# Kernel optimization log

Hardware: AMD Instinct MI355X
Metric: run time of the kernel (lower is better)

The kernel has to match this reference:

```python
import jax, jax.numpy as jnp
import numpy as np
from jax import lax

T, B, D, H = 256, 32, 768, 768


def setup_inputs() -> dict:
    key = jax.random.key(0)
    ks = jax.random.split(key, 8)
    s = 1.0 / np.sqrt(H)
    x = jax.random.normal(ks[0], (T, B, D), dtype=jnp.float32)
    h0 = jax.random.normal(ks[1], (2, B, H), dtype=jnp.float32) * s
    wih_f = jax.random.normal(ks[2], (3 * H, D), dtype=jnp.float32) * s
    whh_f = jax.random.normal(ks[3], (3 * H, H), dtype=jnp.float32) * s
    wih_b = jax.random.normal(ks[4], (3 * H, D), dtype=jnp.float32) * s
    whh_b = jax.random.normal(ks[5], (3 * H, H), dtype=jnp.float32) * s
    bih_f = jnp.zeros((3 * H,), jnp.float32)
    bhh_f = jnp.zeros((3 * H,), jnp.float32)
    bih_b = jnp.zeros((3 * H,), jnp.float32)
    bhh_b = jnp.zeros((3 * H,), jnp.float32)
    # sorted-descending lengths in [T//2, T], as PackedSequence requires
    lengths = jnp.sort(jax.random.randint(ks[6], (B,), T // 2, T + 1))[::-1].astype(jnp.int32)
    return dict(x=x, h0=h0, wih_f=wih_f, whh_f=whh_f, bih_f=bih_f, bhh_f=bhh_f,
                wih_b=wih_b, whh_b=whh_b, bih_b=bih_b, bhh_b=bhh_b, lengths=lengths)


def _gru_scan(x_seq, h0d, Wih, Whh, bih, bhh, mask):
    """Masked GRU scan. x_seq [T,B,D], mask [T,B] bool; hidden frozen where mask is False
    (equivalent to PackedSequence shrinking/growing the active batch)."""
    def step(h, inp):
        x_t, m = inp  # [B,D], [B]
        gx = x_t @ Wih.T + bih          # [B,3H]
        gh = h @ Whh.T + bhh            # [B,3H]
        xr, xz, xn = jnp.split(gx, 3, axis=-1)
        hr, hz, hn = jnp.split(gh, 3, axis=-1)
        r = jax.nn.sigmoid(xr + hr)
        z = jax.nn.sigmoid(xz + hz)
        n = jnp.tanh(xn + r * hn)
        h_new = (1.0 - z) * n + z * h
        h_new = jnp.where(m[:, None], h_new, h)
        return h_new, h_new * m[:, None]  # zero outputs at padded positions
    h_last, outs = lax.scan(step, h0d, (x_seq, mask))
    return outs, h_last


def reference(x, h0, wih_f, whh_f, bih_f, bhh_f, wih_b, whh_b, bih_b, bhh_b, lengths):
    t_idx = jnp.arange(T)[:, None]                 # [T,1]
    mask = t_idx < lengths[None, :]                # [T,B]
    # forward direction
    out_f, h_f = _gru_scan(x, h0[0], wih_f, whh_f, bih_f, bhh_f, mask)
    # reverse direction: flip time, run, flip back
    out_b_rev, h_b = _gru_scan(x[::-1], h0[1], wih_b, whh_b, bih_b, bhh_b, mask[::-1])
    out_b = out_b_rev[::-1]
    outputs = jnp.concatenate([out_f, out_b], axis=-1)  # [T,B,2H], zero beyond length
    h_out = jnp.stack([h_f, h_b], axis=0)                # [2,B,H]
    return outputs, h_out
```

## Files before the change

kernel.cpp:

```cpp
#include <hip/hip_runtime.h>
#include <stdint.h>

typedef unsigned short u16;
typedef unsigned int u32;
typedef _Float16 f16;
typedef __attribute__((ext_vector_type(2))) __fp16 h16x2;
typedef __attribute__((ext_vector_type(8))) _Float16 f16x8;
typedef __attribute__((ext_vector_type(4))) float f32x4;
typedef __attribute__((ext_vector_type(4))) unsigned short u16x4;
typedef __attribute__((ext_vector_type(4))) unsigned int u32x4;

#define T_SEQ  256
#define BATCH  32
#define DIM    768
#define HID    768
#define G3     2304
#define N_ALL  4608
#define NSLICE 48
#define NBLK   96
#define FLAG_STRIDE 32

__device__ __forceinline__ u16 f2h(float f) {
  return __builtin_bit_cast(u16, (f16)f);
}
__device__ __forceinline__ float h2f(u16 h) {
  return (float)__builtin_bit_cast(f16, h);
}

__device__ __forceinline__ f16x8 load_coh16(const u16* p) {
  f16x8 v;
  asm volatile("global_load_dwordx4 %0, %1, off sc0 sc1" : "=v"(v) : "v"(p));
  return v;
}
__device__ __forceinline__ void store_coh16(u16* p, f16x8 v) {
  asm volatile("global_store_dwordx4 %0, %1, off sc0 sc1" :: "v"(p), "v"(v));
}
__device__ __forceinline__ void wait_vm0() {
  asm volatile("s_waitcnt vmcnt(0)" ::: "memory");
}
__device__ __forceinline__ u32 pkrtz(float a, float b) {
  h16x2 p = __builtin_amdgcn_cvt_pkrtz(a, b);
  return __builtin_bit_cast(u32, p);
}
__device__ __forceinline__ f16x8 cvt8(float4 a, float4 b) {
  u32x4 r;
  r.x = pkrtz(a.x, a.y);
  r.y = pkrtz(a.z, a.w);
  r.z = pkrtz(b.x, b.y);
  r.w = pkrtz(b.z, b.w);
  return __builtin_bit_cast(f16x8, r);
}

__global__ void k_cvt(const float* __restrict__ in, u16* __restrict__ out, int n4) {
  int i = blockIdx.x * blockDim.x + threadIdx.x;
  if (i >= n4) return;
  float4 v = ((const float4*)in)[i];
  u16x4 o;
  o[0] = f2h(v.x); o[1] = f2h(v.y); o[2] = f2h(v.z); o[3] = f2h(v.w);
  ((u16x4*)out)[i] = o;
}

__global__ __launch_bounds__(256) void k_gemm(
    const float* __restrict__ X, const float* __restrict__ Wf,
    const float* __restrict__ Wb,
    const float* __restrict__ bihf, const float* __restrict__ bihb,
    u16* __restrict__ gx)
{
  __shared__ __align__(16) u16 As[128 * 32];
  __shared__ __align__(16) u16 Bs[128 * 32];
  const int tid  = threadIdx.x;
  const int lane = tid & 63, wave = tid >> 6;
  const int wm = wave >> 1, wn = wave & 1;
  const int m0 = blockIdx.y * 128;
  const int n0 = blockIdx.x * 128;
  const int lr = lane & 15, lk = lane >> 4;
  f32x4 acc[4][4] = {};
  for (int k0 = 0; k0 < DIM; k0 += 32) {
    __syncthreads();
    #pragma unroll
    for (int i = 0; i < 2; ++i) {
      int cidx = i * 256 + tid;
      int row = cidx >> 2, kk = (cidx & 3) * 8;
      const float* ap = &X[(size_t)(m0 + row) * DIM + k0 + kk];
      *(f16x8*)&As[cidx * 8] = cvt8(*(const float4*)ap, *(const float4*)(ap + 4));
      int n = n0 + row;
      const float* bp = (n < G3 ? &Wf[(size_t)n * DIM] : &Wb[(size_t)(n - G3) * DIM]) + k0 + kk;
      *(f16x8*)&Bs[cidx * 8] = cvt8(*(const float4*)bp, *(const float4*)(bp + 4));
    }
    __syncthreads();
    f16x8 af[4], bfr[4];
    #pragma unroll
    for (int f = 0; f < 4; ++f) {
      af[f]  = *(const f16x8*)&As[(wm * 64 + f * 16 + lr) * 32 + lk * 8];
      bfr[f] = *(const f16x8*)&Bs[(wn * 64 + f * 16 + lr) * 32 + lk * 8];
    }
    #pragma unroll
    for (int fm = 0; fm < 4; ++fm)
      #pragma unroll
      for (int fn = 0; fn < 4; ++fn)
        acc[fm][fn] = __builtin_amdgcn_mfma_f32_16x16x32_f16(af[fm], bfr[fn], acc[fm][fn], 0, 0, 0);
  }
  #pragma unroll
  for (int fm = 0; fm < 4; ++fm)
    #pragma unroll
    for (int fn = 0; fn < 4; ++fn) {
      int n = n0 + wn * 64 + fn * 16 + lr;
      float bias = (n < G3) ? bihf[n] : bihb[n - G3];
      #pragma unroll
      for (int r = 0; r < 4; ++r) {
        int m = m0 + wm * 64 + fm * 16 + lk * 4 + r;
        gx[(size_t)m * N_ALL + n] = f2h(acc[fm][fn][r] + bias);
      }
    }
}

__global__ __launch_bounds__(256, 1) void k_gru(
    const u16* __restrict__ whh,
    const u16* __restrict__ gx,
    const float* __restrict__ h0,
    const float* __restrict__ bhhf, const float* __restrict__ bhhb,
    const int* __restrict__ lengths,
    u16* __restrict__ hbuf,
    float* __restrict__ out, int* __restrict__ flags)
{
  const int blk   = blockIdx.x;
  const int dir   = blk / NSLICE;
  const int slice = blk % NSLICE;
  const int hbase = slice * 16;
  const int tid = threadIdx.x, lane = tid & 63, wave = tid >> 6;
  const int lr = lane & 15, lk = lane >> 4;
  const int c = hbase + lr;
  const int myflag = (lane < 12) ? (dir * NSLICE + wave * 12 + lane) * FLAG_STRIDE : 0;

  __shared__ __align__(16) float part[2][3][2][3][64][4];
  __shared__ __align__(16) u16 hx[32][16];

  f16x8 bw[3][6];
  #pragma unroll
  for (int g = 0; g < 3; ++g)
    #pragma unroll
    for (int ks = 0; ks < 6; ++ks)
      bw[g][ks] = *(const f16x8*)&whh[(size_t)(dir * G3 + g * HID + hbase + lr) * HID
                                      + wave * 192 + ks * 32 + lk * 8];

  float hst[2][4];
  float bh[3] = {0.f, 0.f, 0.f};
  int lenv[2][4];
  u16 g0c[2][4], g1c[2][4], g2c[2][4];
  u16 g0n[2][4], g1n[2][4], g2n[2][4];
  if (wave == 0) {
    #pragma unroll
    for (int m = 0; m < 2; ++m)
      #pragma unroll
      for (int r = 0; r < 4; ++r) {
        int b = m * 16 + lk * 4 + r;
        float h = h0[(size_t)dir * BATCH * HID + (size_t)b * HID + c];
        hst[m][r] = h;
        lenv[m][r] = lengths[b];
        hx[b][lr] = f2h(h);
      }
    const float* bhp = dir ? bhhb : bhhf;
    #pragma unroll
    for (int g = 0; g < 3; ++g) bh[g] = bhp[g * HID + c];
    asm volatile("s_waitcnt lgkmcnt(0)" ::: "memory");
    {
      f16x8 hv = *(const f16x8*)&hx[lane >> 1][(lane & 1) * 8];
      store_coh16(&hbuf[(size_t)(dir * BATCH + (lane >> 1)) * HID + hbase + (lane & 1) * 8], hv);
    }
    wait_vm0();
    if (lane == 0)
      __hip_atomic_store(&flags[blk * FLAG_STRIDE], 1, __ATOMIC_RELAXED, __HIP_MEMORY_SCOPE_AGENT);
    int t0 = dir ? (T_SEQ - 1) : 0;
    #pragma unroll
    for (int m = 0; m < 2; ++m)
      #pragma unroll
      for (int r = 0; r < 4; ++r) {
        int b = m * 16 + lk * 4 + r;
        size_t off = ((size_t)t0 * BATCH + b) * N_ALL + dir * G3 + c;
        g0c[m][r] = gx[off]; g1c[m][r] = gx[off + HID]; g2c[m][r] = gx[off + 2 * HID];
      }
    wait_vm0();
  }
  __syncthreads();

  for (int s = 0; s < T_SEQ; ++s) {
    const int par = s & 1;
    const int t = dir ? (T_SEQ - 1 - s) : s;
    if (wave == 0 && s + 1 < T_SEQ) {
      int t2 = dir ? (T_SEQ - 2 - s) : (s + 1);
      #pragma unroll
      for (int m = 0; m < 2; ++m)
        #pragma unroll
        for (int r = 0; r < 4; ++r) {
          int b = m * 16 + lk * 4 + r;
          size_t off = ((size_t)t2 * BATCH + b) * N_ALL + dir * G3 + c;
          g0n[m][r] = gx[off]; g1n[m][r] = gx[off + HID]; g2n[m][r] = gx[off + 2 * HID];
        }
    }
    __builtin_amdgcn_sched_barrier(0);
    if (lane < 12) {
      while (__hip_atomic_load(&flags[myflag], __ATOMIC_RELAXED, __HIP_MEMORY_SCOPE_AGENT) < s + 1)
        __builtin_amdgcn_s_sleep(1);
    }
    const u16* hb = hbuf + (size_t)(par * 2 + dir) * BATCH * HID;
    f16x8 ah[2][6];
    #pragma unroll
    for (int m = 0; m < 2; ++m)
      #pragma unroll
      for (int ks = 0; ks < 6; ++ks)
        ah[m][ks] = load_coh16(&hb[(size_t)(m * 16 + lr) * HID + wave * 192 + ks * 32 + lk * 8]);
    wait_vm0();
    __builtin_amdgcn_sched_barrier(0);
    f32x4 acc[2][3] = {};
    #pragma unroll
    for (int ks = 0; ks < 6; ++ks)
      #pragma unroll
      for (int m = 0; m < 2; ++m)
        #pragma unroll
        for (int g = 0; g < 3; ++g)
          acc[m][g] = __builtin_amdgcn_mfma_f32_16x16x32_f16(ah[m][ks], bw[g][ks], acc[m][g], 0, 0, 0);
    if (wave != 0) {
      #pragma unroll
      for (int m = 0; m < 2; ++m)
        #pragma unroll
        for (int g = 0; g < 3; ++g)
          *(f32x4*)&part[par][wave - 1][m][g][lane][0] = acc[m][g];
    }
    __syncthreads();
    if (wave == 0) {
      u16* hbn = hbuf + (size_t)((par ^ 1) * 2 + dir) * BATCH * HID;
      float outv[2][4];
      #pragma unroll
      for (int m = 0; m < 2; ++m) {
        f32x4 gh[3];
        #pragma unroll
        for (int g = 0; g < 3; ++g) {
          f32x4 v = acc[m][g];
          #pragma unroll
          for (int w = 0; w < 3; ++w) v += *(const f32x4*)&part[par][w][m][g][lane][0];
          gh[g] = v;
        }
        #pragma unroll
        for (int r = 0; r < 4; ++r) {
          int b = m * 16 + lk * 4 + r;
          float xr = h2f(g0c[m][r]), xz = h2f(g1c[m][r]), xn = h2f(g2c[m][r]);
          float rg = 1.f / (1.f + __expf(-(xr + gh[0][r] + bh[0])));
          float zg = 1.f / (1.f + __expf(-(xz + gh[1][r] + bh[1])));
          float e2 = __expf(2.f * (xn + rg * (gh[2][r] + bh[2])));
          float ng = 1.f - 2.f / (e2 + 1.f);
          float hp = hst[m][r];
          bool msk = t < lenv[m][r];
          float hn = msk ? ((1.f - zg) * ng + zg * hp) : hp;
          hst[m][r] = hn;
          outv[m][r] = msk ? hn : 0.f;
          hx[b][lr] = f2h(hn);
        }
      }
      if (s + 1 < T_SEQ) {
        asm volatile("s_waitcnt lgkmcnt(0)" ::: "memory");
        f16x8 hv = *(const f16x8*)&hx[lane >> 1][(lane & 1) * 8];
        store_coh16(&hbn[(size_t)(lane >> 1) * HID + hbase + (lane & 1) * 8], hv);
        wait_vm0();
        if (lane == 0)
          __hip_atomic_store(&flags[blk * FLAG_STRIDE], s + 2, __ATOMIC_RELAXED, __HIP_MEMORY_SCOPE_AGENT);
      }
      #pragma unroll
      for (int m = 0; m < 2; ++m)
        #pragma unroll
        for (int r = 0; r < 4; ++r) {
          int b = m * 16 + lk * 4 + r;
          __builtin_nontemporal_store(outv[m][r],
              &out[((size_t)t * BATCH + b) * (2 * HID) + (size_t)dir * HID + c]);
        }
      if (s + 1 < T_SEQ) {
        #pragma unroll
        for (int m = 0; m < 2; ++m)
          #pragma unroll
          for (int r = 0; r < 4; ++r) {
            g0c[m][r] = g0n[m][r]; g1c[m][r] = g1n[m][r]; g2c[m][r] = g2n[m][r];
          }
      }
    }
  }
  if (wave == 0) {
    #pragma unroll
    for (int m = 0; m < 2; ++m)
      #pragma unroll
      for (int r = 0; r < 4; ++r) {
        int b = m * 16 + lk * 4 + r;
        out[(size_t)T_SEQ * BATCH * 2 * HID + (size_t)dir * BATCH * HID + (size_t)b * HID + c] = hst[m][r];
      }
  }
}

extern "C" void kernel_launch(void* const* d_in, const int* in_sizes, int n_in,
                              void* d_out, int out_size, void* d_ws, size_t ws_size,
                              hipStream_t stream) {
  const float* x     = (const float*)d_in[0];
  const float* h0    = (const float*)d_in[1];
  const float* wihf  = (const float*)d_in[2];
  const float* whhf  = (const float*)d_in[3];
  const float* bihf  = (const float*)d_in[4];
  const float* bhhf  = (const float*)d_in[5];
  const float* wihb  = (const float*)d_in[6];
  const float* whhb  = (const float*)d_in[7];
  const float* bihb  = (const float*)d_in[8];
  const float* bhhb  = (const float*)d_in[9];
  const int* lengths = (const int*)d_in[10];
  float* out = (float*)d_out;
  char* ws = (char*)d_ws;

  int* flags = (int*)(ws + 0);
  u16* whh_h = (u16*)(ws + 24576);
  u16* hbuf  = (u16*)(ws + 7102464);
  u16* gx    = (u16*)(ws + 7299072);

  k_cvt<<<1728, 256, 0, stream>>>(whhf, whh_h,            442368);
  k_cvt<<<1728, 256, 0, stream>>>(whhb, whh_h + 1769472,  442368);
  (void)hipMemsetAsync(flags, 0, NBLK * FLAG_STRIDE * sizeof(int), stream);
  k_gemm<<<dim3(36, 64), 256, 0, stream>>>(x, wihf, wihb, bihf, bihb, gx);
  k_gru<<<NBLK, 256, 0, stream>>>(whh_h, gx, h0, bhhf, bhhb, lengths, hbuf, out, flags);
}
```

Measured before the change: 1.253 ms.

## Tag hidden-state words with step number and validate data instead of waiting on stores

Each fp16 hidden value is now stored in a 32-bit word whose upper half holds the step tag. Consumers reload any stale 16-byte chunk until every tag matches the expected step, then repack the halves to fp16 for the MFMA. This lets producers drop the vmcnt wait between the hidden-state store and the flag store, removing store latency from the critical path of the cross-block recurrence. The cost is twice the hidden-state traffic, extra repack instructions, and a gx prefetch moved after the output stores. The flag spin is kept, and the retry loop has an iteration cap.

```diff
diff --git a/kernel.cpp b/kernel.cpp
--- a/kernel.cpp
+++ b/kernel.cpp
@@ -27,16 +27,19 @@
   return (float)__builtin_bit_cast(f16, h);
 }
 
-__device__ __forceinline__ f16x8 load_coh16(const u16* p) {
-  f16x8 v;
+__device__ __forceinline__ u32x4 ld_coh4(const u32* p) {
+  u32x4 v;
   asm volatile("global_load_dwordx4 %0, %1, off sc0 sc1" : "=v"(v) : "v"(p));
   return v;
 }
-__device__ __forceinline__ void store_coh16(u16* p, f16x8 v) {
+__device__ __forceinline__ void st_coh16(u32* p, u32x4 v) {
   asm volatile("global_store_dwordx4 %0, %1, off sc0 sc1" :: "v"(p), "v"(v));
 }
 __device__ __forceinline__ void wait_vm0() {
   asm volatile("s_waitcnt vmcnt(0)" ::: "memory");
+}
+__device__ __forceinline__ u32 pk(u32 lo, u32 hi) {
+  return __builtin_amdgcn_perm(hi, lo, 0x05040100u);
 }
 __device__ __forceinline__ u32 pkrtz(float a, float b) {
   h16x2 p = __builtin_amdgcn_cvt_pkrtz(a, b);
@@ -120,7 +123,7 @@
     const float* __restrict__ h0,
     const float* __restrict__ bhhf, const float* __restrict__ bhhb,
     const int* __restrict__ lengths,
-    u16* __restrict__ hbuf,
+    u32* __restrict__ hb,
     float* __restrict__ out, int* __restrict__ flags)
 {
   const int blk   = blockIdx.x;
@@ -133,7 +136,7 @@
   const int myflag = (lane < 12) ? (dir * NSLICE + wave * 12 + lane) * FLAG_STRIDE : 0;
 
   __shared__ __align__(16) float part[2][3][2][3][64][4];
-  __shared__ __align__(16) u16 hx[32][16];
+  __shared__ __align__(16) u32 hx[32][16];
 
   f16x8 bw[3][6];
   #pragma unroll
@@ -147,7 +150,6 @@
   float bh[3] = {0.f, 0.f, 0.f};
   int lenv[2][4];
   u16 g0c[2][4], g1c[2][4], g2c[2][4];
-  u16 g0n[2][4], g1n[2][4], g2n[2][4];
   if (wave == 0) {
     #pragma unroll
     for (int m = 0; m < 2; ++m)
@@ -157,17 +159,18 @@
         float h = h0[(size_t)dir * BATCH * HID + (size_t)b * HID + c];
         hst[m][r] = h;
         lenv[m][r] = lengths[b];
-        hx[b][lr] = f2h(h);
+        hx[b][lr] = (1u << 16) | (u32)f2h(h);
       }
     const float* bhp = dir ? bhhb : bhhf;
     #pragma unroll
     for (int g = 0; g < 3; ++g) bh[g] = bhp[g * HID + c];
     asm volatile("s_waitcnt lgkmcnt(0)" ::: "memory");
     {
-      f16x8 hv = *(const f16x8*)&hx[lane >> 1][(lane & 1) * 8];
-      store_coh16(&hbuf[(size_t)(dir * BATCH + (lane >> 1)) * HID + hbase + (lane & 1) * 8], hv);
-    }
-    wait_vm0();
+      u32* dst0 = hb + (size_t)(0 * 2 + dir) * BATCH * HID;
+      int row = lane >> 1, c8 = (lane & 1) * 8;
+      st_coh16(&dst0[(size_t)row * HID + hbase + c8],     *(const u32x4*)&hx[row][c8]);
+      st_coh16(&dst0[(size_t)row * HID + hbase + c8 + 4], *(const u32x4*)&hx[row][c8 + 4]);
+    }
     if (lane == 0)
       __hip_atomic_store(&flags[blk * FLAG_STRIDE], 1, __ATOMIC_RELAXED, __HIP_MEMORY_SCOPE_AGENT);
     int t0 = dir ? (T_SEQ - 1) : 0;
@@ -179,38 +182,60 @@
         size_t off = ((size_t)t0 * BATCH + b) * N_ALL + dir * G3 + c;
         g0c[m][r] = gx[off]; g1c[m][r] = gx[off + HID]; g2c[m][r] = gx[off + 2 * HID];
       }
-    wait_vm0();
   }
   __syncthreads();
 
   for (int s = 0; s < T_SEQ; ++s) {
     const int par = s & 1;
     const int t = dir ? (T_SEQ - 1 - s) : s;
-    if (wave == 0 && s + 1 < T_SEQ) {
-      int t2 = dir ? (T_SEQ - 2 - s) : (s + 1);
-      #pragma unroll
-      for (int m = 0; m < 2; ++m)
-        #pragma unroll
-        for (int r = 0; r < 4; ++r) {
-          int b = m * 16 + lk * 4 + r;
-          size_t off = ((size_t)t2 * BATCH + b) * N_ALL + dir * G3 + c;
-          g0n[m][r] = gx[off]; g1n[m][r] = gx[off + HID]; g2n[m][r] = gx[off + 2 * HID];
-        }
-    }
-    __builtin_amdgcn_sched_barrier(0);
+    const u32 want = (u32)(s + 1) << 16;
     if (lane < 12) {
       while (__hip_atomic_load(&flags[myflag], __ATOMIC_RELAXED, __HIP_MEMORY_SCOPE_AGENT) < s + 1)
         __builtin_amdgcn_s_sleep(1);
     }
-    const u16* hb = hbuf + (size_t)(par * 2 + dir) * BATCH * HID;
+    const u32* hbp = hb + (size_t)(par * 2 + dir) * BATCH * HID
+                     + (size_t)lr * HID + wave * 192 + lk * 8;
+    u32x4 raw[2][6][2];
+    u32 stale = 0xFFFFFFu;
+    int rounds = 0;
+    do {
+      if (rounds) __builtin_amdgcn_s_sleep(1);
+      #pragma unroll
+      for (int m = 0; m < 2; ++m)
+        #pragma unroll
+        for (int ks = 0; ks < 6; ++ks)
+          #pragma unroll
+          for (int hf = 0; hf < 2; ++hf)
+            if (stale & (1u << ((m * 6 + ks) * 2 + hf)))
+              raw[m][ks][hf] = ld_coh4(hbp + (size_t)m * 16 * HID + ks * 32 + hf * 4);
+      wait_vm0();
+      __builtin_amdgcn_sched_barrier(0);
+      u32 ns = 0;
+      #pragma unroll
+      for (int m = 0; m < 2; ++m)
+        #pragma unroll
+        for (int ks = 0; ks < 6; ++ks)
+          #pragma unroll
+          for (int hf = 0; hf < 2; ++hf)
+            if (stale & (1u << ((m * 6 + ks) * 2 + hf))) {
+              u32x4 v = raw[m][ks][hf];
+              u32 bad = ((v.x ^ want) | (v.y ^ want) | (v.z ^ want) | (v.w ^ want)) & 0xFFFF0000u;
+              if (bad) ns |= 1u << ((m * 6 + ks) * 2 + hf);
+            }
+      stale = ns;
+      ++rounds;
+    } while (__any(stale != 0) && rounds < 2048);
     f16x8 ah[2][6];
     #pragma unroll
     for (int m = 0; m < 2; ++m)
       #pragma unroll
-      for (int ks = 0; ks < 6; ++ks)
-        ah[m][ks] = load_coh16(&hb[(size_t)(m * 16 + lr) * HID + wave * 192 + ks * 32 + lk * 8]);
-    wait_vm0();
-    __builtin_amdgcn_sched_barrier(0);
+      for (int ks = 0; ks < 6; ++ks) {
+        u32x4 lo = raw[m][ks][0], hi = raw[m][ks][1];
+        u32x4 pkd;
+        pkd.x = pk(lo.x, lo.y); pkd.y = pk(lo.z, lo.w);
+        pkd.z = pk(hi.x, hi.y); pkd.w = pk(hi.z, hi.w);
+        ah[m][ks] = __builtin_bit_cast(f16x8, pkd);
+      }
     f32x4 acc[2][3] = {};
     #pragma unroll
     for (int ks = 0; ks < 6; ++ks)
@@ -228,7 +253,6 @@
     }
     __syncthreads();
     if (wave == 0) {
-      u16* hbn = hbuf + (size_t)((par ^ 1) * 2 + dir) * BATCH * HID;
       float outv[2][4];
       #pragma unroll
       for (int m = 0; m < 2; ++m) {
@@ -253,14 +277,15 @@
           float hn = msk ? ((1.f - zg) * ng + zg * hp) : hp;
           hst[m][r] = hn;
           outv[m][r] = msk ? hn : 0.f;
-          hx[b][lr] = f2h(hn);
+          hx[b][lr] = ((u32)(s + 2) << 16) | (u32)f2h(hn);
         }
       }
       if (s + 1 < T_SEQ) {
         asm volatile("s_waitcnt lgkmcnt(0)" ::: "memory");
-        f16x8 hv = *(const f16x8*)&hx[lane >> 1][(lane & 1) * 8];
-        store_coh16(&hbn[(size_t)(lane >> 1) * HID + hbase + (lane & 1) * 8], hv);
-        wait_vm0();
+        u32* dst = hb + (size_t)((par ^ 1) * 2 + dir) * BATCH * HID;
+        int row = lane >> 1, c8 = (lane & 1) * 8;
+        st_coh16(&dst[(size_t)row * HID + hbase + c8],     *(const u32x4*)&hx[row][c8]);
+        st_coh16(&dst[(size_t)row * HID + hbase + c8 + 4], *(const u32x4*)&hx[row][c8 + 4]);
         if (lane == 0)
           __hip_atomic_store(&flags[blk * FLAG_STRIDE], s + 2, __ATOMIC_RELAXED, __HIP_MEMORY_SCOPE_AGENT);
       }
@@ -273,11 +298,14 @@
               &out[((size_t)t * BATCH + b) * (2 * HID) + (size_t)dir * HID + c]);
         }
       if (s + 1 < T_SEQ) {
+        int t2 = dir ? (T_SEQ - 2 - s) : (s + 1);
         #pragma unroll
         for (int m = 0; m < 2; ++m)
           #pragma unroll
           for (int r = 0; r < 4; ++r) {
-            g0c[m][r] = g0n[m][r]; g1c[m][r] = g1n[m][r]; g2c[m][r] = g2n[m][r];
+            int b = m * 16 + lk * 4 + r;
+            size_t off = ((size_t)t2 * BATCH + b) * N_ALL + dir * G3 + c;
+            g0c[m][r] = gx[off]; g1c[m][r] = gx[off + HID]; g2c[m][r] = gx[off + 2 * HID];
           }
       }
     }
@@ -311,13 +339,14 @@
   char* ws = (char*)d_ws;
 
   int* flags = (int*)(ws + 0);
-  u16* whh_h = (u16*)(ws + 24576);
-  u16* hbuf  = (u16*)(ws + 7102464);
-  u16* gx    = (u16*)(ws + 7299072);
+  u32* hbuf2 = (u32*)(ws + 16384);
+  u16* whh_h = (u16*)(ws + 802816);
+  u16* gx    = (u16*)(ws + 7880704);
 
   k_cvt<<<1728, 256, 0, stream>>>(whhf, whh_h,            442368);
   k_cvt<<<1728, 256, 0, stream>>>(whhb, whh_h + 1769472,  442368);
   (void)hipMemsetAsync(flags, 0, NBLK * FLAG_STRIDE * sizeof(int), stream);
+  (void)hipMemsetAsync(hbuf2, 0, 786432, stream);
   k_gemm<<<dim3(36, 64), 256, 0, stream>>>(x, wihf, wihb, bihf, bihb, gx);
-  k_gru<<<NBLK, 256, 0, stream>>>(whh_h, gx, h0, bhhf, bhhb, lengths, hbuf, out, flags);
-}
+  k_gru<<<NBLK, 256, 0, stream>>>(whh_h, gx, h0, bhhf, bhhb, lengths, hbuf2, out, flags);
+}
```

Measured after the change: 1.657 ms, median of 2. 32.2% more time.
